# Performance work log

Measured on AMD Instinct MI355X. Metric: run time of the kernel, lower is better.

The kernel has to match this reference:

```python
import jax, jax.numpy as jnp
import numpy as np

K = 20          # args.k (minu=True)
EPS = 1e-5      # BatchNorm eps
BNS = float(1.0 / np.sqrt(1.0 + EPS))  # eval-mode BN with running_mean=0, running_var=1


def knn_idx(x, k):
    # x: (B, C, N); returns indices of k nearest neighbors (incl. self): (B, N, k)
    xx = jnp.sum(x * x, axis=1)                       # (B, N)
    inner = jnp.einsum('bcn,bcm->bnm', x, x)          # (B, N, N)
    dist = 2.0 * inner - xx[:, :, None] - xx[:, None, :]  # = -||xi - xj||^2
    return jax.lax.top_k(dist, k)[1]


def graph_feature(x, k):
    # x: (B, C, N) -> edge features (B, 2C, N, k) = cat(neighbor - center, center)
    idx = knn_idx(x, k)                               # (B, N, k)
    xt = jnp.transpose(x, (0, 2, 1))                  # (B, N, C)
    feat = jnp.take_along_axis(xt[:, None, :, :], idx[..., None], axis=2)  # (B, N, k, C)
    center = xt[:, :, None, :]
    out = jnp.concatenate([feat - center, jnp.broadcast_to(center, feat.shape)], axis=-1)
    return jnp.transpose(out, (0, 3, 1, 2))


def edge_block(x, w, g, b, k):
    # EdgeConv: gather -> 1x1 conv -> BN(eval) -> LeakyReLU(0.2) -> max over neighbors
    h = graph_feature(x, k)                           # (B, 2C, N, k)
    y = jnp.einsum('bcnk,oc->bonk', h, w)
    y = g[None, :, None, None] * (y * BNS) + b[None, :, None, None]
    y = jax.nn.leaky_relu(y, 0.2)
    return jnp.max(y, axis=-1)                        # (B, O, N)


def _bn1(v, g, b):
    return g * (v * BNS) + b


def setup_inputs() -> dict:
    key = jax.random.key(0)
    ks = jax.random.split(key, 32)
    B, C, N = 16, 6, 1024

    def w(k_, shape):
        return jax.random.normal(k_, shape, jnp.float32) / np.sqrt(shape[1])

    def gm(k_, n):
        return 1.0 + 0.1 * jax.random.normal(k_, (n,), jnp.float32)

    def bt(k_, n):
        return 0.1 * jax.random.normal(k_, (n,), jnp.float32)

    return {
        'x': jax.random.normal(ks[0], (B, C, N), jnp.float32),
        'disc': jax.random.normal(ks[1], (B, 1), jnp.float32),
        'w1': w(ks[2], (64, 12)),   'g1': gm(ks[3], 64),   'b1': bt(ks[4], 64),
        'w2': w(ks[5], (64, 128)),  'g2': gm(ks[6], 64),   'b2': bt(ks[7], 64),
        'w3': w(ks[8], (128, 128)), 'g3': gm(ks[9], 128),  'b3': bt(ks[10], 128),
        'w4': w(ks[11], (256, 256)),'g4': gm(ks[12], 256), 'b4': bt(ks[13], 256),
        'w5': w(ks[14], (1024, 512)),'g5': gm(ks[15], 1024),'b5': bt(ks[16], 1024),
        'wl1': w(ks[17], (256, 2048)),'g6': gm(ks[18], 256),'b6': bt(ks[19], 256),
        'wl2': w(ks[20], (128, 256)),'g7': gm(ks[21], 128),'b7': bt(ks[22], 128),
        'wl21': w(ks[23], (64, 128)),
        'wl22': w(ks[24], (32, 64)),'g8': gm(ks[25], 32), 'b8': bt(ks[26], 32),
        'wl3': w(ks[27], (90, 32)),
    }


def reference(x, disc, w1, g1, b1, w2, g2, b2, w3, g3, b3, w4, g4, b4,
              w5, g5, b5, wl1, g6, b6, wl2, g7, b7, wl21, wl22, g8, b8, wl3):
    # disc is accepted by the original forward but unused
    x1 = edge_block(x, w1, g1, b1, K)                 # (B, 64, N)
    x2 = edge_block(x1, w2, g2, b2, K)                # (B, 64, N)
    x3 = edge_block(x2, w3, g3, b3, K)                # (B, 128, N)
    x4 = edge_block(x3, w4, g4, b4, K)                # (B, 256, N)
    h = jnp.concatenate([x1, x2, x3, x4], axis=1)     # (B, 512, N)
    y = jnp.einsum('bcn,oc->bon', h, w5)              # conv5 1x1
    y = g5[None, :, None] * (y * BNS) + b5[None, :, None]
    y = jax.nn.leaky_relu(y, 0.2)                     # (B, emb, N)
    p = jnp.concatenate([jnp.max(y, axis=2), jnp.mean(y, axis=2)], axis=1)  # (B, 2*emb)
    z = jax.nn.leaky_relu(_bn1(p @ wl1.T, g6, b6), 0.2)
    z = jax.nn.leaky_relu(_bn1(z @ wl2.T, g7, b7), 0.2)
    z = jax.nn.gelu(_bn1((z @ wl21.T) @ wl22.T, g8, b8), approximate=False)
    return z @ wl3.T                                  # (B, 90)
```

## Files before the change

kernel.cpp:

```cpp
#include <hip/hip_runtime.h>
#include <math.h>
#include <float.h>

#define BNS_C 0.9999950000374996f

typedef __bf16 bf8 __attribute__((ext_vector_type(8)));
typedef float f4 __attribute__((ext_vector_type(4)));
union I4BF8 { int4 i; bf8 b; };

static __device__ __forceinline__ unsigned short f2bf(float f) {
    unsigned u = __float_as_uint(f);
    u += 0x7fff + ((u >> 16) & 1);
    return (unsigned short)(u >> 16);
}

__global__ void k_xin_t(const float* __restrict__ x, float* __restrict__ X0, float* __restrict__ xx) {
    int i = blockIdx.x * 256 + threadIdx.x;
    int b = i >> 10, n = i & 1023;
    const float* xb = x + (((size_t)b * 6) << 10) + n;
    float4* o4 = (float4*)(X0 + ((size_t)i << 3));
    float v0 = xb[0], v1 = xb[1 << 10], v2 = xb[2 << 10];
    float v3 = xb[3 << 10], v4 = xb[4 << 10], v5 = xb[5 << 10];
    o4[0] = make_float4(v0, v1, v2, v3);
    o4[1] = make_float4(v4, v5, 0.f, 0.f);
    xx[i] = v0*v0 + v1*v1 + v2*v2 + v3*v3 + v4*v4 + v5*v5;
}

__global__ __launch_bounds__(256) void k_gram2(const float* __restrict__ X, const float* __restrict__ xx,
                                               float* __restrict__ D, int Cp, int b0) {
    int z = blockIdx.z, b = b0 + z;
    int n0 = blockIdx.y * 64, m0 = blockIdx.x * 64;
    __shared__ float As[64][33], Bs[64][33];
    int tid = threadIdx.x;
    int ti = tid & 15, tj = tid >> 4;
    float acc[4][4] = {};
    const float* Xb = X + (((size_t)b) << 10) * Cp;
    for (int c0 = 0; c0 < Cp; c0 += 32) {
        for (int e = tid; e < 2048; e += 256) {
            int row = e >> 5, cc = e & 31, c = c0 + cc;
            float a = 0.f, bb = 0.f;
            if (c < Cp) {
                a  = Xb[(size_t)(n0 + row) * Cp + c];
                bb = Xb[(size_t)(m0 + row) * Cp + c];
            }
            As[row][cc] = a; Bs[row][cc] = bb;
        }
        __syncthreads();
#pragma unroll 8
        for (int cc = 0; cc < 32; ++cc) {
            float xv[4], yv[4];
#pragma unroll
            for (int a = 0; a < 4; ++a) xv[a] = As[tj + 16 * a][cc];
#pragma unroll
            for (int q = 0; q < 4; ++q) yv[q] = Bs[ti + 16 * q][cc];
#pragma unroll
            for (int a = 0; a < 4; ++a)
#pragma unroll
                for (int q = 0; q < 4; ++q) acc[a][q] += xv[a] * yv[q];
        }
        __syncthreads();
    }
#pragma unroll
    for (int a = 0; a < 4; ++a) {
        int n = n0 + tj + 16 * a;
        float xn = xx[(b << 10) + n];
#pragma unroll
        for (int q = 0; q < 4; ++q) {
            int m = m0 + ti + 16 * q;
            D[((size_t)((z << 10) + n) << 10) + m] = 2.f * acc[a][q] - xn - xx[(b << 10) + m];
        }
    }
}

__global__ __launch_bounds__(256) void k_topk(const float* __restrict__ D, int* __restrict__ idxo, int b0) {
    const int K = 20;
    int lane = threadIdx.x & 63;
    int rl = blockIdx.x * 4 + (threadIdx.x >> 6);
    const float* row = D + ((size_t)rl << 10);
    float d[16];
#pragma unroll
    for (int j = 0; j < 16; ++j) d[j] = row[lane + 64 * j];
    int rg = (b0 << 10) + rl;
    for (int it = 0; it < K; ++it) {
        float bv = d[0]; int bj = 0;
#pragma unroll
        for (int j = 1; j < 16; ++j) if (d[j] > bv) { bv = d[j]; bj = j; }
        int bm = lane + (bj << 6);
        for (int off = 32; off > 0; off >>= 1) {
            float ov = __shfl_down(bv, off);
            int   om = __shfl_down(bm, off);
            if (ov > bv || (ov == bv && om < bm)) { bv = ov; bm = om; }
        }
        bm = __shfl(bm, 0);
        if (lane == 0) idxo[rg * K + it] = bm;
        if ((bm & 63) == lane) d[bm >> 6] = -FLT_MAX;
    }
}

__global__ __launch_bounds__(256) void k_uv(const float* __restrict__ X, const float* __restrict__ w,
                                            float* __restrict__ V, float* __restrict__ U,
                                            int Cp, int C, int O) {
    int n0 = blockIdx.x * 64, o0 = blockIdx.y * 64, b = blockIdx.z;
    __shared__ float Xs[64][33], Was[64][33], Wds[64][33];
    int tid = threadIdx.x, ti = tid & 15, tj = tid >> 4;
    float accv[4][4] = {}, accu[4][4] = {};
    const float* Xb = X + (((size_t)b) << 10) * Cp;
    int W2 = 2 * C;
    for (int c0 = 0; c0 < Cp; c0 += 32) {
        for (int e = tid; e < 2048; e += 256) {
            int row = e >> 5, cc = e & 31, c = c0 + cc;
            Xs[row][cc] = (c < Cp) ? Xb[(size_t)(n0 + row) * Cp + c] : 0.f;
            float wa = 0.f, wd = 0.f;
            if (c < C) {
                float a_ = w[(size_t)(o0 + row) * W2 + c];
                float b_ = w[(size_t)(o0 + row) * W2 + C + c];
                wa = a_; wd = b_ - a_;
            }
            Was[row][cc] = wa; Wds[row][cc] = wd;
        }
        __syncthreads();
#pragma unroll 8
        for (int cc = 0; cc < 32; ++cc) {
            float xv[4], av[4], dv[4];
#pragma unroll
            for (int a = 0; a < 4; ++a) xv[a] = Xs[tj + 16 * a][cc];
#pragma unroll
            for (int q = 0; q < 4; ++q) { av[q] = Was[ti + 16 * q][cc]; dv[q] = Wds[ti + 16 * q][cc]; }
#pragma unroll
            for (int a = 0; a < 4; ++a)
#pragma unroll
                for (int q = 0; q < 4; ++q) { accv[a][q] += xv[a] * av[q]; accu[a][q] += xv[a] * dv[q]; }
        }
        __syncthreads();
    }
#pragma unroll
    for (int a = 0; a < 4; ++a) {
        int n = n0 + tj + 16 * a;
#pragma unroll
        for (int q = 0; q < 4; ++q) {
            int o = o0 + ti + 16 * q;
            size_t oi = ((size_t)((b << 10) + n)) * O + o;
            V[oi] = accv[a][q]; U[oi] = accu[a][q];
        }
    }
}

__global__ __launch_bounds__(256) void k_gmax(const float* __restrict__ V, const float* __restrict__ U,
                                              const int* __restrict__ idx,
                                              const float* __restrict__ gg, const float* __restrict__ bb,
                                              float* __restrict__ Xo, float* __restrict__ xx,
                                              unsigned short* __restrict__ HB, int coff, int O) {
    __shared__ float sxx[4];
    int tid = threadIdx.x;
    int Tn = 256 / O;
    int j = tid / O, o = tid - j * O;
    int pt = blockIdx.x * Tn + j;
    int b = pt >> 10;
    float uv = U[(size_t)pt * O + o];
    float gv = gg[o], bv = bb[o];
    const int* ip = idx + (size_t)pt * 20;
    float mx = -FLT_MAX;
    for (int k = 0; k < 20; ++k) {
        int m = ip[k] & 1023;
        float vv = V[(size_t)((b << 10) + m) * O + o];
        float y = gv * ((vv + uv) * BNS_C) + bv;
        y = y > 0.f ? y : 0.2f * y;
        mx = fmaxf(mx, y);
    }
    Xo[(size_t)pt * O + o] = mx;
    HB[(size_t)pt * 512 + coff + o] = f2bf(mx);
    float s = mx * mx;
#pragma unroll
    for (int off = 32; off; off >>= 1) s += __shfl_down(s, off);
    int wid = tid >> 6, lane = tid & 63;
    if (lane == 0) sxx[wid] = s;
    __syncthreads();
    if (o == 0) {
        int Wpp = O >> 6;
        float t = 0.f;
        for (int w = 0; w < Wpp; ++w) t += sxx[j * Wpp + w];
        xx[pt] = t;
    }
}

__global__ __launch_bounds__(256) void k_final_mfma(const unsigned short* __restrict__ HB,
                                                    const float* __restrict__ w5,
                                                    const float* __restrict__ g5,
                                                    const float* __restrict__ b5,
                                                    float* __restrict__ p) {
    int b = blockIdx.y;
    int wv = threadIdx.x >> 6, lane = threadIdx.x & 63;
    int r = lane & 15, q = lane >> 4;
    int o = blockIdx.x * 64 + wv * 16 + r;
    bf8 Bfr[16];
    const float* wrow = w5 + (size_t)o * 512 + q * 8;
#pragma unroll
    for (int s = 0; s < 16; ++s) {
        float4 f0 = *(const float4*)(wrow + s * 32);
        float4 f1 = *(const float4*)(wrow + s * 32 + 4);
        I4BF8 u_;
        u_.i.x = f2bf(f0.x) | ((unsigned)f2bf(f0.y) << 16);
        u_.i.y = f2bf(f0.z) | ((unsigned)f2bf(f0.w) << 16);
        u_.i.z = f2bf(f1.x) | ((unsigned)f2bf(f1.y) << 16);
        u_.i.w = f2bf(f1.z) | ((unsigned)f2bf(f1.w) << 16);
        Bfr[s] = u_.b;
    }
    float gb = g5[o] * BNS_C, bv = b5[o];
    const unsigned short* HBb = HB + ((((size_t)b) << 10)) * 512 + q * 8;
    float mx = -FLT_MAX, sm = 0.f;
    for (int g = 0; g < 16; ++g) {
        const unsigned short* a0 = HBb + (size_t)(g * 64 +  0 + r) * 512;
        const unsigned short* a1 = HBb + (size_t)(g * 64 + 16 + r) * 512;
        const unsigned short* a2 = HBb + (size_t)(g * 64 + 32 + r) * 512;
        const unsigned short* a3 = HBb + (size_t)(g * 64 + 48 + r) * 512;
        f4 C0 = {0.f, 0.f, 0.f, 0.f}, C1 = C0, C2 = C0, C3 = C0;
#pragma unroll
        for (int s = 0; s < 16; ++s) {
            I4BF8 A0, A1, A2, A3;
            A0.i = *(const int4*)(a0 + s * 32);
            A1.i = *(const int4*)(a1 + s * 32);
            A2.i = *(const int4*)(a2 + s * 32);
            A3.i = *(const int4*)(a3 + s * 32);
            C0 = __builtin_amdgcn_mfma_f32_16x16x32_bf16(A0.b, Bfr[s], C0, 0, 0, 0);
            C1 = __builtin_amdgcn_mfma_f32_16x16x32_bf16(A1.b, Bfr[s], C1, 0, 0, 0);
            C2 = __builtin_amdgcn_mfma_f32_16x16x32_bf16(A2.b, Bfr[s], C2, 0, 0, 0);
            C3 = __builtin_amdgcn_mfma_f32_16x16x32_bf16(A3.b, Bfr[s], C3, 0, 0, 0);
        }
#pragma unroll
        for (int e = 0; e < 4; ++e) {
            float y0 = gb * C0[e] + bv; y0 = y0 > 0.f ? y0 : 0.2f * y0; mx = fmaxf(mx, y0); sm += y0;
            float y1 = gb * C1[e] + bv; y1 = y1 > 0.f ? y1 : 0.2f * y1; mx = fmaxf(mx, y1); sm += y1;
            float y2 = gb * C2[e] + bv; y2 = y2 > 0.f ? y2 : 0.2f * y2; mx = fmaxf(mx, y2); sm += y2;
            float y3 = gb * C3[e] + bv; y3 = y3 > 0.f ? y3 : 0.2f * y3; mx = fmaxf(mx, y3); sm += y3;
        }
    }
    mx = fmaxf(mx, __shfl_down(mx, 32)); sm += __shfl_down(sm, 32);
    mx = fmaxf(mx, __shfl_down(mx, 16)); sm += __shfl_down(sm, 16);
    if (q == 0) {
        p[b * 2048 + o] = mx;
        p[b * 2048 + 1024 + o] = sm * (1.f / 1024.f);
    }
}

__global__ __launch_bounds__(256) void k_fc2(const float* __restrict__ in, const float* __restrict__ w,
                                             const float* __restrict__ gg, const float* __restrict__ bb,
                                             float* __restrict__ out,
                                             int R, int C, int O, int act) {
    int gw = blockIdx.x * 4 + (threadIdx.x >> 6);
    int lane = threadIdx.x & 63;
    if (gw >= R * O) return;
    int r = gw / O, o = gw - r * O;
    const float* ir = in + (size_t)r * C;
    const float* wr = w + (size_t)o * C;
    float s = 0.f;
    for (int c = lane; c < C; c += 64) s += ir[c] * wr[c];
#pragma unroll
    for (int off = 32; off; off >>= 1) s += __shfl_down(s, off);
    if (lane == 0) {
        float y = s;
        if (gg) y = gg[o] * (s * BNS_C) + bb[o];
        if (act == 1) y = y > 0.f ? y : 0.2f * y;
        else if (act == 2) y = 0.5f * y * (1.f + erff(y * 0.70710678118654752f));
        out[gw] = y;
    }
}

extern "C" void kernel_launch(void* const* d_in, const int* in_sizes, int n_in,
                              void* d_out, int out_size, void* d_ws, size_t ws_size,
                              hipStream_t stream) {
    typedef const float* fp;
    fp x  = (fp)d_in[0];
    fp w1 = (fp)d_in[2],  g1 = (fp)d_in[3],  b1 = (fp)d_in[4];
    fp w2 = (fp)d_in[5],  g2 = (fp)d_in[6],  b2 = (fp)d_in[7];
    fp w3 = (fp)d_in[8],  g3 = (fp)d_in[9],  b3 = (fp)d_in[10];
    fp w4 = (fp)d_in[11], g4 = (fp)d_in[12], b4 = (fp)d_in[13];
    fp w5 = (fp)d_in[14], g5 = (fp)d_in[15], b5 = (fp)d_in[16];
    fp wl1 = (fp)d_in[17], g6 = (fp)d_in[18], b6 = (fp)d_in[19];
    fp wl2 = (fp)d_in[20], g7 = (fp)d_in[21], b7 = (fp)d_in[22];
    fp wl21 = (fp)d_in[23], wl22 = (fp)d_in[24];
    fp g8 = (fp)d_in[25], b8 = (fp)d_in[26], wl3 = (fp)d_in[27];

    char* ws = (char*)d_ws;
    size_t off = 0;
    auto alloc = [&](size_t floats) { float* p_ = (float*)(ws + off); off += floats * 4; off = (off + 255) & ~(size_t)255; return p_; };
    float* X0  = alloc(131072);
    float* X1  = alloc(1048576);
    float* X2  = alloc(1048576);
    float* X3  = alloc(2097152);
    float* X4  = alloc(4194304);
    float* xx  = alloc(16384);
    int*   nbr = (int*)alloc(327680);
    unsigned short* HB = (unsigned short*)alloc(4194304);
    float* p   = alloc(32768);
    float* z1  = alloc(4096);
    float* z2  = alloc(2048);
    float* zt  = alloc(1024);
    float* z3  = alloc(512);
    size_t poolAvail = (ws_size > off) ? (ws_size - off) / 4 : 0;
    int fullD = poolAvail >= 16777216;
    float* pool = alloc(fullD ? 16777216 : 8388608);

    float* D = pool;
    float* V = pool;
    float* U = pool + 4194304;

    k_xin_t<<<64, 256, 0, stream>>>(x, X0, xx);

    struct Blk { const float* Xin; int Cp, C, O, coff; const float *w, *g, *b; float* Xout; };
    Blk blks[4] = {
        {X0, 8,   6,   64,  0,   w1, g1, b1, X1},
        {X1, 64,  64,  64,  64,  w2, g2, b2, X2},
        {X2, 64,  64,  128, 128, w3, g3, b3, X3},
        {X3, 128, 128, 256, 256, w4, g4, b4, X4},
    };
    for (int i = 0; i < 4; ++i) {
        const Blk& B_ = blks[i];
        if (fullD) {
            k_gram2<<<dim3(16, 16, 16), 256, 0, stream>>>(B_.Xin, xx, D, B_.Cp, 0);
            k_topk<<<4096, 256, 0, stream>>>(D, nbr, 0);
        } else {
            for (int b0 = 0; b0 < 16; b0 += 8) {
                k_gram2<<<dim3(16, 16, 8), 256, 0, stream>>>(B_.Xin, xx, D, B_.Cp, b0);
                k_topk<<<2048, 256, 0, stream>>>(D, nbr, b0);
            }
        }
        k_uv<<<dim3(16, B_.O / 64, 16), 256, 0, stream>>>(B_.Xin, B_.w, V, U, B_.Cp, B_.C, B_.O);
        int Tn = 256 / B_.O;
        k_gmax<<<16384 / Tn, 256, 0, stream>>>(V, U, nbr, B_.g, B_.b, B_.Xout, xx, HB, B_.coff, B_.O);
    }

    k_final_mfma<<<dim3(16, 16), 256, 0, stream>>>(HB, w5, g5, b5, p);

    k_fc2<<<(16 * 256 + 3) / 4, 256, 0, stream>>>(p,  wl1, g6, b6, z1, 16, 2048, 256, 1);
    k_fc2<<<(16 * 128 + 3) / 4, 256, 0, stream>>>(z1, wl2, g7, b7, z2, 16, 256, 128, 1);
    k_fc2<<<(16 * 64  + 3) / 4, 256, 0, stream>>>(z2, wl21, nullptr, nullptr, zt, 16, 128, 64, 0);
    k_fc2<<<(16 * 32  + 3) / 4, 256, 0, stream>>>(zt, wl22, g8, b8, z3, 16, 64, 32, 2);
    k_fc2<<<(16 * 90  + 3) / 4, 256, 0, stream>>>(z3, wl3, nullptr, nullptr, (float*)d_out, 16, 32, 90, 0);
}
```

Before: 1.002 ms.

## Split final conv over point tiles and fuse small FC layers into one kernel

New measurement: 1.035 ms. +3.3%, slower.

```diff
diff --git a/kernel.cpp b/kernel.cpp
--- a/kernel.cpp
+++ b/kernel.cpp
@@ -187,11 +187,12 @@
                                                     const float* __restrict__ w5,
                                                     const float* __restrict__ g5,
                                                     const float* __restrict__ b5,
-                                                    float* __restrict__ p) {
-    int b = blockIdx.y;
+                                                    float* __restrict__ pp) {
+    int b = blockIdx.x;
+    int nt = blockIdx.z;
     int wv = threadIdx.x >> 6, lane = threadIdx.x & 63;
     int r = lane & 15, q = lane >> 4;
-    int o = blockIdx.x * 64 + wv * 16 + r;
+    int o = blockIdx.y * 64 + wv * 16 + r;
     bf8 Bfr[16];
     const float* wrow = w5 + (size_t)o * 512 + q * 8;
 #pragma unroll
@@ -206,9 +207,9 @@
         Bfr[s] = u_.b;
     }
     float gb = g5[o] * BNS_C, bv = b5[o];
-    const unsigned short* HBb = HB + ((((size_t)b) << 10)) * 512 + q * 8;
+    const unsigned short* HBb = HB + ((((size_t)b) << 10) + (nt << 8)) * 512 + q * 8;
     float mx = -FLT_MAX, sm = 0.f;
-    for (int g = 0; g < 16; ++g) {
+    for (int g = 0; g < 4; ++g) {
         const unsigned short* a0 = HBb + (size_t)(g * 64 +  0 + r) * 512;
         const unsigned short* a1 = HBb + (size_t)(g * 64 + 16 + r) * 512;
         const unsigned short* a2 = HBb + (size_t)(g * 64 + 32 + r) * 512;
@@ -237,9 +238,22 @@
     mx = fmaxf(mx, __shfl_down(mx, 32)); sm += __shfl_down(sm, 32);
     mx = fmaxf(mx, __shfl_down(mx, 16)); sm += __shfl_down(sm, 16);
     if (q == 0) {
-        p[b * 2048 + o] = mx;
-        p[b * 2048 + 1024 + o] = sm * (1.f / 1024.f);
-    }
+        float* pb = pp + (size_t)(nt * 16 + b) * 2048;
+        pb[o] = mx;
+        pb[1024 + o] = sm;
+    }
+}
+
+__global__ void k_pfinal(const float* __restrict__ pp, float* __restrict__ p) {
+    int i = blockIdx.x * 256 + threadIdx.x;
+    int b = i >> 10, o = i & 1023;
+    float mx = -FLT_MAX, sm = 0.f;
+    for (int nt = 0; nt < 4; ++nt) {
+        const float* q = pp + (size_t)(nt * 16 + b) * 2048;
+        mx = fmaxf(mx, q[o]); sm += q[1024 + o];
+    }
+    p[b * 2048 + o] = mx;
+    p[b * 2048 + 1024 + o] = sm * (1.f / 1024.f);
 }
 
 __global__ __launch_bounds__(256) void k_fc2(const float* __restrict__ in, const float* __restrict__ w,
@@ -262,6 +276,58 @@
         if (act == 1) y = y > 0.f ? y : 0.2f * y;
         else if (act == 2) y = 0.5f * y * (1.f + erff(y * 0.70710678118654752f));
         out[gw] = y;
+    }
+}
+
+__global__ __launch_bounds__(256) void k_fc_tail(const float* __restrict__ z1,
+                                                 const float* __restrict__ wl2, const float* __restrict__ g7, const float* __restrict__ b7,
+                                                 const float* __restrict__ wl21,
+                                                 const float* __restrict__ wl22, const float* __restrict__ g8, const float* __restrict__ b8,
+                                                 const float* __restrict__ wl3,
+                                                 float* __restrict__ out) {
+    __shared__ float L0[4096];
+    __shared__ float L1[2048];
+    __shared__ float L2[1024];
+    __shared__ float L3[512];
+    int tid = threadIdx.x;
+    for (int i = tid; i < 4096; i += 256) L0[i] = z1[i];
+    __syncthreads();
+    for (int idx = tid; idx < 2048; idx += 256) {
+        int o = idx >> 4, r = idx & 15;
+        const float* wr = wl2 + (size_t)o * 256;
+        const float* ir = L0 + r * 256;
+        float s = 0.f;
+        for (int c = 0; c < 256; ++c) s += ir[c] * wr[c];
+        float y = g7[o] * (s * BNS_C) + b7[o];
+        L1[r * 128 + o] = y > 0.f ? y : 0.2f * y;
+    }
+    __syncthreads();
+    for (int idx = tid; idx < 1024; idx += 256) {
+        int o = idx >> 4, r = idx & 15;
+        const float* wr = wl21 + (size_t)o * 128;
+        const float* ir = L1 + r * 128;
+        float s = 0.f;
+        for (int c = 0; c < 128; ++c) s += ir[c] * wr[c];
+        L2[r * 64 + o] = s;
+    }
+    __syncthreads();
+    for (int idx = tid; idx < 512; idx += 256) {
+        int o = idx >> 4, r = idx & 15;
+        const float* wr = wl22 + (size_t)o * 64;
+        const float* ir = L2 + r * 64;
+        float s = 0.f;
+        for (int c = 0; c < 64; ++c) s += ir[c] * wr[c];
+        float y = g8[o] * (s * BNS_C) + b8[o];
+        L3[r * 32 + o] = 0.5f * y * (1.f + erff(y * 0.70710678118654752f));
+    }
+    __syncthreads();
+    for (int idx = tid; idx < 1440; idx += 256) {
+        int o = idx / 16, r = idx & 15;
+        const float* wr = wl3 + (size_t)o * 32;
+        const float* ir = L3 + r * 32;
+        float s = 0.f;
+        for (int c = 0; c < 32; ++c) s += ir[c] * wr[c];
+        out[r * 90 + o] = s;
     }
 }
 
@@ -291,11 +357,9 @@
     float* xx  = alloc(16384);
     int*   nbr = (int*)alloc(327680);
     unsigned short* HB = (unsigned short*)alloc(4194304);
+    float* pp  = alloc(131072);
     float* p   = alloc(32768);
     float* z1  = alloc(4096);
-    float* z2  = alloc(2048);
-    float* zt  = alloc(1024);
-    float* z3  = alloc(512);
     size_t poolAvail = (ws_size > off) ? (ws_size - off) / 4 : 0;
     int fullD = poolAvail >= 16777216;
     float* pool = alloc(fullD ? 16777216 : 8388608);
@@ -329,11 +393,9 @@
         k_gmax<<<16384 / Tn, 256, 0, stream>>>(V, U, nbr, B_.g, B_.b, B_.Xout, xx, HB, B_.coff, B_.O);
     }
 
-    k_final_mfma<<<dim3(16, 16), 256, 0, stream>>>(HB, w5, g5, b5, p);
-
-    k_fc2<<<(16 * 256 + 3) / 4, 256, 0, stream>>>(p,  wl1, g6, b6, z1, 16, 2048, 256, 1);
-    k_fc2<<<(16 * 128 + 3) / 4, 256, 0, stream>>>(z1, wl2, g7, b7, z2, 16, 256, 128, 1);
-    k_fc2<<<(16 * 64  + 3) / 4, 256, 0, stream>>>(z2, wl21, nullptr, nullptr, zt, 16, 128, 64, 0);
-    k_fc2<<<(16 * 32  + 3) / 4, 256, 0, stream>>>(zt, wl22, g8, b8, z3, 16, 64, 32, 2);
-    k_fc2<<<(16 * 90  + 3) / 4, 256, 0, stream>>>(z3, wl3, nullptr, nullptr, (float*)d_out, 16, 32, 90, 0);
-}
+    k_final_mfma<<<dim3(16, 16, 4), 256, 0, stream>>>(HB, w5, g5, b5, pp);
+    k_pfinal<<<64, 256, 0, stream>>>(pp, p);
+
+    k_fc2<<<(16 * 256 + 3) / 4, 256, 0, stream>>>(p, wl1, g6, b6, z1, 16, 2048, 256, 1);
+    k_fc_tail<<<1, 256, 0, stream>>>(z1, wl2, g7, b7, wl21, wl22, g8, b8, wl3, (float*)d_out);
+}
```
